# Kernel optimization log

Measured on AMD Instinct MI355X. Metric: run time of the kernel, lower is better.

The kernel has to match this reference:

```python
import jax, jax.numpy as jnp
import numpy as np

B, C, H, W = 32, 256, 32, 32   # batch, channels (inplanes==planes), spatial
E = 8                          # num_experts
EPS = 1e-5                     # BatchNorm eps


def setup_inputs() -> dict:
    key = jax.random.key(0)
    ks = jax.random.split(key, 6)
    s = 0.05
    return {
        "x": jax.random.normal(ks[0], (B, C, H, W), dtype=jnp.float32),
        # router: GAP -> Linear(C, E) -> sigmoid
        "router_w": jax.random.normal(ks[1], (E, C), dtype=jnp.float32) * s,
        "router_b": jnp.zeros((E,), dtype=jnp.float32),
        # expert kernel banks for the two CondConv2d layers (OIHW per expert)
        "w1": jax.random.normal(ks[2], (E, C, C, 3, 3), dtype=jnp.float32) * s,
        "w2": jax.random.normal(ks[3], (E, C, C, 3, 3), dtype=jnp.float32) * s,
        # BatchNorm (eval mode: running stats) params for bn1/bn2
        "g1": jnp.ones((C,), jnp.float32), "b1": jnp.zeros((C,), jnp.float32),
        "m1": jnp.zeros((C,), jnp.float32), "v1": jnp.ones((C,), jnp.float32),
        "g2": jnp.ones((C,), jnp.float32), "b2": jnp.zeros((C,), jnp.float32),
        "m2": jnp.zeros((C,), jnp.float32), "v2": jnp.ones((C,), jnp.float32),
    }


def _bn(x, g, b, m, v):
    # eval-mode BatchNorm over channel dim 1
    scale = (g * jax.lax.rsqrt(v + EPS))[None, :, None, None]
    shift = (b - m * g * jax.lax.rsqrt(v + EPS))[None, :, None, None]
    return x * scale + shift


def _cond_conv(x, w_bank, r):
    # x: [B,C,H,W]; w_bank: [E,O,I,3,3]; r: [B,E]
    # combine expert kernels per sample, then per-sample 3x3 conv (pad=1, stride=1)
    k = jnp.einsum('be,eoihw->boihw', r, w_bank)  # [B,O,I,3,3]

    def one(xb, kb):
        return jax.lax.conv_general_dilated(
            xb[None], kb, window_strides=(1, 1), padding=[(1, 1), (1, 1)],
            dimension_numbers=('NCHW', 'OIHW', 'NCHW'))[0]

    return jax.vmap(one)(x, k)  # [B,O,H,W]


def reference(x, router_w, router_b, w1, w2, g1, b1, m1, v1, g2, b2, m2, v2):
    # BasicRouter: global average pool -> linear -> sigmoid
    r = jax.nn.sigmoid(jnp.mean(x, axis=(2, 3)) @ router_w.T + router_b)  # [B,E]
    # drop_expert is identity in eval mode (training=False)
    out = jax.nn.relu(_bn(_cond_conv(x, w1, r), g1, b1, m1, v1))
    out = _bn(_cond_conv(out, w2, r), g2, b2, m2, v2)
    return jax.nn.relu(out + x)  # identity residual (stride=1, inplanes==planes)
```

## Files before the change

### kernel.cpp

```cpp
#include <hip/hip_runtime.h>

typedef unsigned short ushort_t;
typedef __attribute__((ext_vector_type(8))) __bf16 bf16x8;
typedef __attribute__((ext_vector_type(4))) float f32x4;
typedef __attribute__((ext_vector_type(4))) int i32x4;
typedef __attribute__((ext_vector_type(4))) unsigned short u16x4;

#define BN_EPS 1e-5f
#define EPAD 136

__device__ __forceinline__ ushort_t f2bf(float f) {
    union { float f; unsigned u; } v; v.f = f;
    unsigned r = v.u + 0x7FFFu + ((v.u >> 16) & 1u);
    return (ushort_t)(r >> 16);
}
__device__ __forceinline__ float bf2f(ushort_t h) {
    union { unsigned u; float f; } v; v.u = ((unsigned)h) << 16; return v.f;
}

__device__ __forceinline__ void async_cp16(const ushort_t* g, ushort_t* l) {
    __builtin_amdgcn_global_load_lds(
        (const __attribute__((address_space(1))) unsigned int*)g,
        (__attribute__((address_space(3))) unsigned int*)l, 16, 0, 0);
}

__global__ void transpose_gap_kernel(const float* __restrict__ x, ushort_t* __restrict__ xt,
                                     float* __restrict__ gapsum) {
    __shared__ float tile[32][33];
    int b = blockIdx.z, c0 = blockIdx.y * 32, p0 = blockIdx.x * 32;
    int tx = threadIdx.x & 31, ty = threadIdx.x >> 5;
    float ps[4];
    #pragma unroll
    for (int i = 0; i < 4; ++i) {
        int c = ty + i * 8;
        float v = x[((long)b * 256 + c0 + c) * 1024 + p0 + tx];
        tile[c][tx] = v;
        ps[i] = v;
    }
    #pragma unroll
    for (int off = 16; off; off >>= 1)
        #pragma unroll
        for (int i = 0; i < 4; ++i) ps[i] += __shfl_down(ps[i], off, 32);
    if (tx == 0)
        #pragma unroll
        for (int i = 0; i < 4; ++i) atomicAdd(&gapsum[b * 256 + c0 + ty + i * 8], ps[i]);
    __syncthreads();
    #pragma unroll
    for (int i = 0; i < 4; ++i) {
        int p = ty + i * 8;
        xt[((long)b * 1024 + p0 + p) * 256 + c0 + tx] = f2bf(tile[tx][p]);
    }
}

__global__ void router_linear_kernel(const float* __restrict__ gapsum, const float* __restrict__ rw,
                                     const float* __restrict__ rb, float* __restrict__ r) {
    int t = threadIdx.x, b = t >> 3, e = t & 7;
    float s = 0.f;
    for (int c = 0; c < 256; ++c) s += gapsum[b * 256 + c] * rw[e * 256 + c];
    r[t] = 1.f / (1.f + expf(-(s * (1.f / 1024.f) + rb[e])));
}

__global__ void combine_kernel(const float* __restrict__ w, const float* __restrict__ r,
                               ushort_t* __restrict__ ko) {
    int g = blockIdx.x * 256 + threadIdx.x;
    int b0 = blockIdx.y * 8;
    float wv[8][9];
    #pragma unroll
    for (int e = 0; e < 8; ++e)
        #pragma unroll
        for (int p = 0; p < 9; ++p)
            wv[e][p] = w[((long)e * 65536 + g) * 9 + p];
    for (int bb = 0; bb < 8; ++bb) {
        int b = b0 + bb;
        float rv[8];
        #pragma unroll
        for (int e = 0; e < 8; ++e) rv[e] = r[b * 8 + e];
        #pragma unroll
        for (int p = 0; p < 9; ++p) {
            float s = 0.f;
            #pragma unroll
            for (int e = 0; e < 8; ++e) s += rv[e] * wv[e][p];
            ko[((long)(b * 9 + p)) * 65536 + g] = f2bf(s);
        }
    }
}

template <int MODE>
__global__ __launch_bounds__(256, 2) void gemm_conv(
    const ushort_t* __restrict__ xin,
    const ushort_t* __restrict__ kbank,
    void* __restrict__ outp,
    const float* __restrict__ gam, const float* __restrict__ bet,
    const float* __restrict__ mu, const float* __restrict__ var,
    const ushort_t* __restrict__ residt) {
    __shared__ ushort_t smem[29440];
    ushort_t* ldsB = smem;
    ushort_t* ldsA = smem + 13056;

    const int t = threadIdx.x;
    const int lane = t & 63;
    const int lane15 = lane & 15;
    const int quad = lane >> 4;
    const int wv = t >> 6;
    const int id = blockIdx.x;
    const int q  = id >> 3;
    const int mt = q & 1;
    const int nt = (q >> 1) & 7;
    const int b  = (id & 7) + ((q >> 4) << 3);
    const int h0 = nt * 4;
    const int p0 = nt * 128;
    const int mw0 = (wv >> 1) * 64;
    const int nw0 = (wv & 1) * 64;
    const int wbase = t & ~63;

    f32x4 acc[4][4];
    #pragma unroll
    for (int i = 0; i < 4; ++i)
        #pragma unroll
        for (int j = 0; j < 4; ++j) acc[i][j] = 0.f;

    if (t < 96) {
        int rix = t >> 3, j = t & 7;
        int pi = (rix >> 1) * 34 + (rix & 1) * 33;
        i32x4 z = 0;
        *(i32x4*)(&ldsB[(pi * 8 + j) * 8]) = z;
    }
    if (nt == 0) { i32x4 z = 0; *(i32x4*)(&ldsB[(8 + t) * 8]) = z; }
    if (nt == 7) { i32x4 z = 0; *(i32x4*)(&ldsB[((5 * 34 + 1) * 8 + t) * 8]) = z; }

    const long xbase = (long)b * 1024 * 256;
    const long kbase = (long)b * 9 * 65536;

    auto stageB = [&](int kc) {
        #pragma unroll
        for (int hh = 0; hh < 6; ++hh) {
            int hg = h0 + hh - 1;
            if (hg < 0 || hg >= 32) continue;
            int ww = t >> 3;
            int pi = hh * 34 + 1 + ww;
            int jd = (t & 7) ^ (pi & 7);
            async_cp16(xin + xbase + (long)(hg * 32 + ww) * 256 + kc * 64 + jd * 8,
                       ldsB + ((hh * 34 + 1) * 8 + wbase) * 8);
        }
    };
    auto stageA = [&](int kc, int pos, int buf) {
        const ushort_t* srcA = kbank + kbase + (long)pos * 65536 + (long)mt * 32768 + kc * 64;
        ushort_t* base = ldsA + buf * 8192;
        #pragma unroll
        for (int it = 0; it < 4; ++it) {
            int s = it * 256 + t;
            int row = s >> 3;
            int k8 = (s & 7) ^ (row & 7);
            async_cp16(srcA + (long)row * 256 + k8 * 8, base + (it * 256 + wbase) * 8);
        }
    };

    stageB(0);
    stageA(0, 0, 0);
    __syncthreads();

    int par = 0;
    for (int kc = 0; kc < 4; ++kc) {
        for (int pos = 0; pos < 9; ++pos) {
            if (!(kc == 3 && pos == 8)) {
                int nk = kc, np = pos + 1;
                if (np == 9) { np = 0; ++nk; }
                stageA(nk, np, par ^ 1);
            }
            const int dh = pos / 3 - 1, dw = pos % 3 - 1;
            const ushort_t* ab = ldsA + par * 8192;
            #pragma unroll
            for (int kb = 0; kb < 2; ++kb) {
                int jk = kb * 4 + quad;
                bf16x8 af[4], bfr[4];
                #pragma unroll
                for (int mf = 0; mf < 4; ++mf) {
                    int row = mw0 + mf * 16 + lane15;
                    af[mf] = *(const bf16x8*)(ab + (row * 8 + (jk ^ (row & 7))) * 8);
                }
                #pragma unroll
                for (int nf = 0; nf < 4; ++nf) {
                    int n = nw0 + nf * 16 + lane15;
                    int pi = ((n >> 5) + 1 + dh) * 34 + (n & 31) + 1 + dw;
                    bfr[nf] = *(const bf16x8*)(&ldsB[(pi * 8 + (jk ^ (pi & 7))) * 8]);
                }
                #pragma unroll
                for (int mf = 0; mf < 4; ++mf)
                    #pragma unroll
                    for (int nf = 0; nf < 4; ++nf)
                        acc[mf][nf] = __builtin_amdgcn_mfma_f32_16x16x32_bf16(af[mf], bfr[nf], acc[mf][nf], 0, 0, 0);
            }
            __syncthreads();
            if (pos == 8 && kc < 3) { stageB(kc + 1); __syncthreads(); }
            par ^= 1;
        }
    }

    u16x4 rres[4][4];
    if (MODE == 1) {
        #pragma unroll
        for (int mf = 0; mf < 4; ++mf)
            #pragma unroll
            for (int nf = 0; nf < 4; ++nf) {
                int p = p0 + nw0 + nf * 16 + lane15;
                int cb = mt * 128 + mw0 + mf * 16 + quad * 4;
                rres[mf][nf] = *(const u16x4*)(residt + ((long)b * 1024 + p) * 256 + cb);
            }
    }

    float sc[4][4], sh[4][4];
    #pragma unroll
    for (int mf = 0; mf < 4; ++mf)
        #pragma unroll
        for (int i = 0; i < 4; ++i) {
            int c = mt * 128 + mw0 + mf * 16 + quad * 4 + i;
            float s = gam[c] * rsqrtf(var[c] + BN_EPS);
            sc[mf][i] = s;
            sh[mf][i] = bet[c] - mu[c] * s;
        }

    if (MODE == 0) {
        __syncthreads();
        ushort_t* ldsE = smem;
        #pragma unroll
        for (int mf = 0; mf < 4; ++mf)
            #pragma unroll
            for (int nf = 0; nf < 4; ++nf) {
                int pl = nw0 + nf * 16 + lane15;
                int cb = mw0 + mf * 16 + quad * 4;
                u16x4 pk;
                #pragma unroll
                for (int i = 0; i < 4; ++i) {
                    float v = acc[mf][nf][i] * sc[mf][i] + sh[mf][i];
                    pk[i] = f2bf(fmaxf(v, 0.f));
                }
                *(u16x4*)(&ldsE[pl * EPAD + cb]) = pk;
            }
        __syncthreads();
        ushort_t* op = (ushort_t*)outp;
        #pragma unroll
        for (int it = 0; it < 8; ++it) {
            int s = t + it * 256;
            int row = s >> 4, l16 = s & 15;
            i32x4 v = *(i32x4*)(&ldsE[row * EPAD + l16 * 8]);
            *(i32x4*)(op + ((long)b * 1024 + p0 + row) * 256 + mt * 128 + l16 * 8) = v;
        }
    } else {
        float* op = (float*)outp;
        #pragma unroll
        for (int mf = 0; mf < 4; ++mf)
            #pragma unroll
            for (int nf = 0; nf < 4; ++nf) {
                int p = p0 + nw0 + nf * 16 + lane15;
                #pragma unroll
                for (int i = 0; i < 4; ++i) {
                    int c = mt * 128 + mw0 + mf * 16 + quad * 4 + i;
                    float v = acc[mf][nf][i] * sc[mf][i] + sh[mf][i] + bf2f(rres[mf][nf][i]);
                    op[((long)b * 256 + c) * 1024 + p] = fmaxf(v, 0.f);
                }
            }
    }
}

extern "C" void kernel_launch(void* const* d_in, const int* in_sizes, int n_in,
                              void* d_out, int out_size, void* d_ws, size_t ws_size,
                              hipStream_t stream) {
    const float* x  = (const float*)d_in[0];
    const float* rw = (const float*)d_in[1];
    const float* rb = (const float*)d_in[2];
    const float* w1 = (const float*)d_in[3];
    const float* w2 = (const float*)d_in[4];
    const float* g1 = (const float*)d_in[5];
    const float* b1 = (const float*)d_in[6];
    const float* m1 = (const float*)d_in[7];
    const float* v1 = (const float*)d_in[8];
    const float* g2 = (const float*)d_in[9];
    const float* b2 = (const float*)d_in[10];
    const float* m2 = (const float*)d_in[11];
    const float* v2 = (const float*)d_in[12];

    const size_t GAP_OFF = 4096;
    const size_t XT_OFF  = 36864;
    const size_t O1_OFF  = XT_OFF + (size_t)16777216;
    const size_t KB_OFF  = O1_OFF + (size_t)16777216;
    const size_t NEED    = KB_OFF + (size_t)32 * 9 * 65536 * 2;
    if (ws_size < NEED) return;

    char* ws = (char*)d_ws;
    float* r       = (float*)ws;
    float* gapsum  = (float*)(ws + GAP_OFF);
    ushort_t* xt   = (ushort_t*)(ws + XT_OFF);
    ushort_t* o1   = (ushort_t*)(ws + O1_OFF);
    ushort_t* kbuf = (ushort_t*)(ws + KB_OFF);

    hipMemsetAsync(gapsum, 0, 32768, stream);
    transpose_gap_kernel<<<dim3(32, 8, 32), 256, 0, stream>>>(x, xt, gapsum);
    router_linear_kernel<<<1, 256, 0, stream>>>(gapsum, rw, rb, r);
    combine_kernel<<<dim3(256, 4), 256, 0, stream>>>(w1, r, kbuf);
    gemm_conv<0><<<512, 256, 0, stream>>>(xt, kbuf, (void*)o1, g1, b1, m1, v1, nullptr);
    combine_kernel<<<dim3(256, 4), 256, 0, stream>>>(w2, r, kbuf);
    gemm_conv<1><<<512, 256, 0, stream>>>(o1, kbuf, d_out, g2, b2, m2, v2, xt);
}
```

Baseline: 258.3 us.

## Restructure conv GEMM main loop with explicit waitcnt barriers and combine grid

The GEMM main loop now issues the next A-tile async copy, waits only on the older loads via vmcnt, then barriers, loads all LDS fragments for both k-sub-blocks into registers, waits on lgkmcnt and barriers again before running the MFMAs at raised priority. The B-stage reload is moved to overlap with the MFMA phase. The intent is to reduce barrier stalls and let global→LDS copies overlap compute. Separately, the combine kernel now loops over all 32 batches per thread instead of splitting across 4 grid rows, which avoids reloading expert weights four times but reduces parallelism. The hand-written waitcnt counts and the stageB timing relative to readers of ldsB carry correctness risk.

```diff
diff --git a/kernel.cpp b/kernel.cpp
--- a/kernel.cpp
+++ b/kernel.cpp
@@ -8,6 +8,11 @@
 
 #define BN_EPS 1e-5f
 #define EPAD 136
+
+#define BAR()    __builtin_amdgcn_s_barrier()
+#define VMCNT4() asm volatile("s_waitcnt vmcnt(4)" ::: "memory")
+#define VMCNT0() asm volatile("s_waitcnt vmcnt(0)" ::: "memory")
+#define LGKM0()  asm volatile("s_waitcnt lgkmcnt(0)" ::: "memory")
 
 __device__ __forceinline__ ushort_t f2bf(float f) {
     union { float f; unsigned u; } v; v.f = f;
@@ -63,15 +68,13 @@
 __global__ void combine_kernel(const float* __restrict__ w, const float* __restrict__ r,
                                ushort_t* __restrict__ ko) {
     int g = blockIdx.x * 256 + threadIdx.x;
-    int b0 = blockIdx.y * 8;
     float wv[8][9];
     #pragma unroll
     for (int e = 0; e < 8; ++e)
         #pragma unroll
         for (int p = 0; p < 9; ++p)
             wv[e][p] = w[((long)e * 65536 + g) * 9 + p];
-    for (int bb = 0; bb < 8; ++bb) {
-        int b = b0 + bb;
+    for (int b = 0; b < 32; ++b) {
         float rv[8];
         #pragma unroll
         for (int e = 0; e < 8; ++e) rv[e] = r[b * 8 + e];
@@ -162,36 +165,49 @@
     int par = 0;
     for (int kc = 0; kc < 4; ++kc) {
         for (int pos = 0; pos < 9; ++pos) {
-            if (!(kc == 3 && pos == 8)) {
+            const bool last = (kc == 3 && pos == 8);
+            if (!last) {
                 int nk = kc, np = pos + 1;
                 if (np == 9) { np = 0; ++nk; }
                 stageA(nk, np, par ^ 1);
-            }
+                VMCNT4();
+            } else {
+                VMCNT0();
+            }
+            BAR();
+
             const int dh = pos / 3 - 1, dw = pos % 3 - 1;
             const ushort_t* ab = ldsA + par * 8192;
+            bf16x8 af[2][4], bv[2][4];
             #pragma unroll
             for (int kb = 0; kb < 2; ++kb) {
                 int jk = kb * 4 + quad;
-                bf16x8 af[4], bfr[4];
                 #pragma unroll
                 for (int mf = 0; mf < 4; ++mf) {
                     int row = mw0 + mf * 16 + lane15;
-                    af[mf] = *(const bf16x8*)(ab + (row * 8 + (jk ^ (row & 7))) * 8);
+                    af[kb][mf] = *(const bf16x8*)(ab + (row * 8 + (jk ^ (row & 7))) * 8);
                 }
                 #pragma unroll
                 for (int nf = 0; nf < 4; ++nf) {
                     int n = nw0 + nf * 16 + lane15;
                     int pi = ((n >> 5) + 1 + dh) * 34 + (n & 31) + 1 + dw;
-                    bfr[nf] = *(const bf16x8*)(&ldsB[(pi * 8 + (jk ^ (pi & 7))) * 8]);
+                    bv[kb][nf] = *(const bf16x8*)(&ldsB[(pi * 8 + (jk ^ (pi & 7))) * 8]);
                 }
+            }
+            LGKM0();
+            BAR();
+
+            if (pos == 8 && kc < 3) stageB(kc + 1);
+
+            __builtin_amdgcn_s_setprio(1);
+            #pragma unroll
+            for (int kb = 0; kb < 2; ++kb)
                 #pragma unroll
                 for (int mf = 0; mf < 4; ++mf)
                     #pragma unroll
                     for (int nf = 0; nf < 4; ++nf)
-                        acc[mf][nf] = __builtin_amdgcn_mfma_f32_16x16x32_bf16(af[mf], bfr[nf], acc[mf][nf], 0, 0, 0);
-            }
-            __syncthreads();
-            if (pos == 8 && kc < 3) { stageB(kc + 1); __syncthreads(); }
+                        acc[mf][nf] = __builtin_amdgcn_mfma_f32_16x16x32_bf16(af[kb][mf], bv[kb][nf], acc[mf][nf], 0, 0, 0);
+            __builtin_amdgcn_s_setprio(0);
             par ^= 1;
         }
     }
@@ -296,8 +312,8 @@
     hipMemsetAsync(gapsum, 0, 32768, stream);
     transpose_gap_kernel<<<dim3(32, 8, 32), 256, 0, stream>>>(x, xt, gapsum);
     router_linear_kernel<<<1, 256, 0, stream>>>(gapsum, rw, rb, r);
-    combine_kernel<<<dim3(256, 4), 256, 0, stream>>>(w1, r, kbuf);
+    combine_kernel<<<dim3(256), 256, 0, stream>>>(w1, r, kbuf);
     gemm_conv<0><<<512, 256, 0, stream>>>(xt, kbuf, (void*)o1, g1, b1, m1, v1, nullptr);
-    combine_kernel<<<dim3(256, 4), 256, 0, stream>>>(w2, r, kbuf);
+    combine_kernel<<<dim3(256), 256, 0, stream>>>(w2, r, kbuf);
     gemm_conv<1><<<512, 256, 0, stream>>>(o1, kbuf, d_out, g2, b2, m2, v2, xt);
 }
```

Result: slower. 287.0 us (+11.1%).
